# Performance work log

Measured on AMD Instinct MI355X. Metric: run time of the kernel, lower is better.

## Reference

```python
import jax, jax.numpy as jnp
import numpy as np

BN_EPS = 1e-5  # torch BatchNorm1d default


def setup_inputs() -> dict:
    key = jax.random.key(0)
    k = jax.random.split(key, 5)
    B, D, L = 4096, 4096, 4  # batch, width, num layers (3 hidden + 1 output)
    x = jax.random.normal(k[0], (B, D), dtype=jnp.float32)
    # Per-layer Linear weights stored as [L, in, out]; scaled like xavier-ish init.
    W = jax.random.normal(k[1], (L, D, D), dtype=jnp.float32) * (1.0 / np.sqrt(D))
    b = jax.random.normal(k[2], (L, D), dtype=jnp.float32) * 0.01
    gamma = jax.random.uniform(k[3], (L, D), dtype=jnp.float32, minval=0.5, maxval=1.5)
    beta = jax.random.normal(k[4], (L, D), dtype=jnp.float32) * 0.1
    return {"x": x, "W": W, "b": b, "gamma": gamma, "beta": beta}


def _layer(h, W_l, b_l, gamma_l, beta_l):
    # one big GEMM replaces the per-neuron GEMV loop + stack
    h = h @ W_l + b_l  # [B, out]
    # BatchNorm1d, training mode: biased batch stats over the batch dim
    mu = jnp.mean(h, axis=0)
    var = jnp.var(h, axis=0)
    h = (h - mu) * jax.lax.rsqrt(var + BN_EPS) * gamma_l + beta_l
    return jax.nn.relu(h)


def reference(x, W, b, gamma, beta):
    out = x
    for l in range(W.shape[0]):  # small fixed layer count
        out = _layer(out, W[l], b[l], gamma[l], beta[l])
    # nn.Softmax(dim=0): softmax over the batch dimension, as in the original
    return jax.nn.softmax(out, axis=0)
```

## Files before the change

### kernel.cpp

```cpp
#include <hip/hip_runtime.h>
#include <stdint.h>

#define DIMD 4096
#define DIMB 4096
#define NLAYER 4
#define NT (DIMD / 64)

typedef unsigned short u16;
typedef __attribute__((ext_vector_type(4))) float f32x4;
typedef __attribute__((ext_vector_type(8))) __bf16 bf16x8;

__device__ __forceinline__ u16 f2bf(float f) {
    union { float f; uint32_t u; } v; v.f = f;
    return (u16)((v.u + 0x7fffu + ((v.u >> 16) & 1u)) >> 16);
}

__global__ void k_cvt(const float* __restrict__ in, u16* __restrict__ out) {
    int i = (blockIdx.x * 256 + threadIdx.x) * 4;
    float4 v = *reinterpret_cast<const float4*>(in + i);
    ushort4 r;
    r.x = f2bf(v.x); r.y = f2bf(v.y); r.z = f2bf(v.z); r.w = f2bf(v.w);
    *reinterpret_cast<ushort4*>(out + i) = r;
}

__global__ void k_trans(const float* __restrict__ W, u16* __restrict__ Wt) {
    __shared__ float tile[64][65];
    const int t = threadIdx.x;
    const int n0 = blockIdx.x * 64, k0 = blockIdx.y * 64;
    const int kr = t >> 4, c4 = (t & 15) * 4;
    #pragma unroll
    for (int r = 0; r < 4; ++r) {
        float4 v = *reinterpret_cast<const float4*>(W + (size_t)(k0 + kr + r * 16) * DIMD + n0 + c4);
        tile[kr + r * 16][c4 + 0] = v.x;
        tile[kr + r * 16][c4 + 1] = v.y;
        tile[kr + r * 16][c4 + 2] = v.z;
        tile[kr + r * 16][c4 + 3] = v.w;
    }
    __syncthreads();
    const int nr = t >> 4, k4 = (t & 15) * 4;
    #pragma unroll
    for (int r = 0; r < 4; ++r) {
        int n = nr + r * 16;
        ushort4 o;
        o.x = f2bf(tile[k4 + 0][n]);
        o.y = f2bf(tile[k4 + 1][n]);
        o.z = f2bf(tile[k4 + 2][n]);
        o.w = f2bf(tile[k4 + 3][n]);
        *reinterpret_cast<ushort4*>(Wt + (size_t)(n0 + n) * DIMD + k0 + k4) = o;
    }
}

#define GLD(g, l) __builtin_amdgcn_global_load_lds( \
    (__attribute__((address_space(1))) void*)(g),   \
    (__attribute__((address_space(3))) void*)(l), 16, 0, 0)

__global__ __launch_bounds__(512, 2) void k_gemm(
        const u16* __restrict__ A, const u16* __restrict__ Bt,
        const float* __restrict__ bias, float* __restrict__ C,
        float* __restrict__ csum, float* __restrict__ csum2) {
    __shared__ __attribute__((aligned(16))) u16 As[2 * 256 * 64];
    __shared__ __attribute__((aligned(16))) u16 Bs[2 * 256 * 64];
    const int tid = threadIdx.x;
    const int lane = tid & 63, wv = tid >> 6;
    const int wm = wv >> 2, wn = wv & 3;
    const int bm = blockIdx.y, bn = blockIdx.x;
    const int lr = lane & 15, lk = lane >> 4;

    const int r0 = tid >> 3;
    const int cswz = (tid & 7) ^ (r0 & 7);
    const u16* gA = A  + (size_t)(bm * 256 + r0) * DIMD + cswz * 8;
    const u16* gB = Bt + (size_t)(bn * 256 + r0) * DIMD + cswz * 8;

#define STAGE_A(h, t, buf) do { \
    const u16* _s = gA + (size_t)(h) * 128 * DIMD + (size_t)(t) * 64; \
    u16* _d = As + (buf) * 16384 + (h) * 8192 + wv * 512; \
    GLD(_s, _d); GLD(_s + (size_t)64 * DIMD, _d + 4096); \
} while (0)
#define STAGE_B(h, t, buf) do { \
    const u16* _s = gB + (size_t)(h) * 128 * DIMD + (size_t)(t) * 64; \
    u16* _d = Bs + (buf) * 16384 + (h) * 8192 + wv * 512; \
    GLD(_s, _d); GLD(_s + (size_t)64 * DIMD, _d + 4096); \
} while (0)

    int aoff[4][2], boff[2][2];
    #pragma unroll
    for (int mf = 0; mf < 4; ++mf)
        #pragma unroll
        for (int ks = 0; ks < 2; ++ks) {
            int row = wm * 128 + mf * 16 + lr;
            aoff[mf][ks] = row * 64 + ((ks * 4 + lk) ^ (row & 7)) * 8;
        }
    #pragma unroll
    for (int nf = 0; nf < 2; ++nf)
        #pragma unroll
        for (int ks = 0; ks < 2; ++ks) {
            int row = wn * 64 + nf * 16 + lr;
            boff[nf][ks] = row * 64 + ((ks * 4 + lk) ^ (row & 7)) * 8;
        }

    f32x4 acc[8][4] = {};
    bf16x8 a[4][2], b0[2][2], b1[2][2];

    STAGE_B(0, 0, 0); STAGE_B(1, 0, 0); STAGE_A(0, 0, 0); STAGE_A(1, 0, 0);
    STAGE_B(0, 1, 1); STAGE_B(1, 1, 1); STAGE_A(0, 1, 1); STAGE_A(1, 1, 1);
    asm volatile("s_waitcnt vmcnt(8)" ::: "memory");
    __builtin_amdgcn_s_barrier();

    for (int t = 0; t < NT; ++t) {
        const int cur = t & 1;
        const u16* Ab = As + cur * 16384;
        const u16* Bb = Bs + cur * 16384;
        const bool pf = (t + 2 < NT);

        #pragma unroll
        for (int mf = 0; mf < 4; ++mf)
            #pragma unroll
            for (int ks = 0; ks < 2; ++ks)
                a[mf][ks] = *reinterpret_cast<const bf16x8*>(Ab + aoff[mf][ks]);
        #pragma unroll
        for (int nf = 0; nf < 2; ++nf)
            #pragma unroll
            for (int ks = 0; ks < 2; ++ks)
                b0[nf][ks] = *reinterpret_cast<const bf16x8*>(Bb + boff[nf][ks]);
        __builtin_amdgcn_s_barrier();
        asm volatile("s_waitcnt lgkmcnt(0)" ::: "memory");
        __builtin_amdgcn_s_setprio(1);
        #pragma unroll
        for (int mf = 0; mf < 4; ++mf)
            #pragma unroll
            for (int nf = 0; nf < 2; ++nf)
                #pragma unroll
                for (int ks = 0; ks < 2; ++ks)
                    acc[mf][nf] = __builtin_amdgcn_mfma_f32_16x16x32_bf16(
                        a[mf][ks], b0[nf][ks], acc[mf][nf], 0, 0, 0);
        __builtin_amdgcn_s_setprio(0);
        __builtin_amdgcn_s_barrier();

        #pragma unroll
        for (int nf = 0; nf < 2; ++nf)
            #pragma unroll
            for (int ks = 0; ks < 2; ++ks)
                b1[nf][ks] = *reinterpret_cast<const bf16x8*>(Bb + 2048 + boff[nf][ks]);
        __builtin_amdgcn_s_barrier();
        asm volatile("s_waitcnt lgkmcnt(0)" ::: "memory");
        __builtin_amdgcn_s_setprio(1);
        #pragma unroll
        for (int mf = 0; mf < 4; ++mf)
            #pragma unroll
            for (int nf = 0; nf < 2; ++nf)
                #pragma unroll
                for (int ks = 0; ks < 2; ++ks)
                    acc[mf][2 + nf] = __builtin_amdgcn_mfma_f32_16x16x32_bf16(
                        a[mf][ks], b1[nf][ks], acc[mf][2 + nf], 0, 0, 0);
        __builtin_amdgcn_s_setprio(0);
        __builtin_amdgcn_s_barrier();

        #pragma unroll
        for (int mf = 0; mf < 4; ++mf)
            #pragma unroll
            for (int ks = 0; ks < 2; ++ks)
                a[mf][ks] = *reinterpret_cast<const bf16x8*>(Ab + 4096 + aoff[mf][ks]);
        if (pf) { STAGE_B(0, t + 2, cur); STAGE_B(1, t + 2, cur); }
        __builtin_amdgcn_s_barrier();
        asm volatile("s_waitcnt lgkmcnt(0)" ::: "memory");
        __builtin_amdgcn_s_setprio(1);
        #pragma unroll
        for (int mf = 0; mf < 4; ++mf)
            #pragma unroll
            for (int nf = 0; nf < 2; ++nf)
                #pragma unroll
                for (int ks = 0; ks < 2; ++ks)
                    acc[4 + mf][2 + nf] = __builtin_amdgcn_mfma_f32_16x16x32_bf16(
                        a[mf][ks], b1[nf][ks], acc[4 + mf][2 + nf], 0, 0, 0);
        __builtin_amdgcn_s_setprio(0);
        __builtin_amdgcn_s_barrier();

        if (pf) { STAGE_A(0, t + 2, cur); STAGE_A(1, t + 2, cur); }
        __builtin_amdgcn_s_setprio(1);
        #pragma unroll
        for (int mf = 0; mf < 4; ++mf)
            #pragma unroll
            for (int nf = 0; nf < 2; ++nf)
                #pragma unroll
                for (int ks = 0; ks < 2; ++ks)
                    acc[4 + mf][nf] = __builtin_amdgcn_mfma_f32_16x16x32_bf16(
                        a[mf][ks], b0[nf][ks], acc[4 + mf][nf], 0, 0, 0);
        __builtin_amdgcn_s_setprio(0);
        if (pf) asm volatile("s_waitcnt vmcnt(8)" ::: "memory");
        else    asm volatile("s_waitcnt vmcnt(0)" ::: "memory");
        __builtin_amdgcn_s_barrier();
    }

    #pragma unroll
    for (int nh = 0; nh < 2; ++nh)
        #pragma unroll
        for (int nf = 0; nf < 2; ++nf) {
            int n = nh * 2 + nf;
            int col = bn * 256 + wn * 64 + nh * 32 + nf * 16 + lr;
            float bv = bias[col];
            float s1 = 0.f, s2 = 0.f;
            #pragma unroll
            for (int m = 0; m < 8; ++m) {
                int rbase = bm * 256 + wm * 128 + (m >> 2) * 64 + (m & 3) * 16 + lk * 4;
                #pragma unroll
                for (int r = 0; r < 4; ++r) {
                    float v = acc[m][n][r] + bv;
                    C[(size_t)(rbase + r) * DIMD + col] = v;
                    s1 += v; s2 += v * v;
                }
            }
            s1 += __shfl_xor(s1, 16); s1 += __shfl_xor(s1, 32);
            s2 += __shfl_xor(s2, 16); s2 += __shfl_xor(s2, 32);
            if (lk == 0) {
                atomicAdd(&csum[col], s1);
                atomicAdd(&csum2[col], s2);
            }
        }
#undef STAGE_A
#undef STAGE_B
}

__global__ void k_bnfin(float* __restrict__ sum, float* __restrict__ sum2,
                        const float* __restrict__ gamma, const float* __restrict__ beta) {
    int j = blockIdx.x * 256 + threadIdx.x;
    float mu = sum[j] * (1.0f / DIMB);
    float var = sum2[j] * (1.0f / DIMB) - mu * mu;
    float rstd = rsqrtf(var + 1e-5f);
    float s = gamma[j] * rstd;
    sum[j] = s;
    sum2[j] = beta[j] - mu * s;
}

__global__ void k_norm(const float* __restrict__ H, const float* __restrict__ s,
                       const float* __restrict__ t, u16* __restrict__ o) {
    int j = blockIdx.x * 256 + threadIdx.x;
    int i0 = blockIdx.y * 128;
    float sj = s[j], tj = t[j];
    for (int i = i0; i < i0 + 128; ++i) {
        float v = fmaxf(H[(size_t)i * DIMD + j] * sj + tj, 0.0f);
        o[(size_t)i * DIMD + j] = f2bf(v);
    }
}

__global__ void k_normexp(float* __restrict__ H, const float* __restrict__ s,
                          const float* __restrict__ t, float* __restrict__ esum) {
    int j = blockIdx.x * 256 + threadIdx.x;
    int i0 = blockIdx.y * 128;
    float sj = s[j], tj = t[j];
    float acc = 0.f;
    for (int i = i0; i < i0 + 128; ++i) {
        float v = fmaxf(H[(size_t)i * DIMD + j] * sj + tj, 0.0f);
        float e = __expf(v);
        H[(size_t)i * DIMD + j] = e;
        acc += e;
    }
    atomicAdd(&esum[j], acc);
}

__global__ void k_div(float* __restrict__ H, const float* __restrict__ esum) {
    int i = (blockIdx.x * 256 + threadIdx.x) * 4;
    float4 v = *reinterpret_cast<const float4*>(H + i);
    const float4 e = *reinterpret_cast<const float4*>(esum + (i & (DIMD - 1)));
    v.x /= e.x; v.y /= e.y; v.z /= e.z; v.w /= e.w;
    *reinterpret_cast<float4*>(H + i) = v;
}

extern "C" void kernel_launch(void* const* d_in, const int* in_sizes, int n_in,
                              void* d_out, int out_size, void* d_ws, size_t ws_size,
                              hipStream_t stream) {
    (void)in_sizes; (void)n_in; (void)out_size; (void)ws_size;
    const float* x     = (const float*)d_in[0];
    const float* W     = (const float*)d_in[1];
    const float* b     = (const float*)d_in[2];
    const float* gamma = (const float*)d_in[3];
    const float* beta  = (const float*)d_in[4];
    float* out = (float*)d_out;

    char* ws = (char*)d_ws;
    u16*  Abf   = (u16*)ws;
    u16*  Wt    = (u16*)(ws + (size_t)32 * 1024 * 1024);
    float* stats = (float*)(ws + (size_t)64 * 1024 * 1024);
    hipMemsetAsync(stats, 0, (4 * 8192 + 4096) * sizeof(float), stream);

    k_cvt<<<DIMB * DIMD / 1024, 256, 0, stream>>>(x, Abf);

    for (int l = 0; l < NLAYER; ++l) {
        k_trans<<<dim3(64, 64), 256, 0, stream>>>(W + (size_t)l * DIMD * DIMD, Wt);
        float* sum = stats + l * 8192;
        float* sum2 = sum + 4096;
        k_gemm<<<dim3(16, 16), 512, 0, stream>>>(Abf, Wt, b + l * DIMD, out, sum, sum2);
        k_bnfin<<<16, 256, 0, stream>>>(sum, sum2, gamma + l * DIMD, beta + l * DIMD);
        if (l < NLAYER - 1)
            k_norm<<<dim3(16, 32), 256, 0, stream>>>(out, sum, sum2, Abf);
        else
            k_normexp<<<dim3(16, 32), 256, 0, stream>>>(out, sum, sum2, stats + 32768);
    }
    k_div<<<DIMB * DIMD / 1024, 256, 0, stream>>>(out, stats + 32768);
}
```

Measured before the change: 733.7 us.

## Switch GEMM to 32x32x16 MFMA, batch weight transposes, fold BN finalize into norm

The GEMM inner loop now uses 32x32x16 bf16 MFMA instructions instead of 16x16x32. The LDS fragment offsets and the epilogue row mapping are rewritten to match the larger accumulator layout. The intent is fewer MFMA issues and fewer LDS reads per FLOP. All four weight transposes are merged into one 3D launch writing a larger workspace, and the BN finalize kernel is folded into the norm kernels to cut launches. The cost is more workspace memory and a recomputed finalize in every norm block.

```diff
diff --git a/kernel.cpp b/kernel.cpp
--- a/kernel.cpp
+++ b/kernel.cpp
@@ -7,7 +7,7 @@
 #define NT (DIMD / 64)
 
 typedef unsigned short u16;
-typedef __attribute__((ext_vector_type(4))) float f32x4;
+typedef __attribute__((ext_vector_type(16))) float f32x16;
 typedef __attribute__((ext_vector_type(8))) __bf16 bf16x8;
 
 __device__ __forceinline__ u16 f2bf(float f) {
@@ -26,11 +26,12 @@
 __global__ void k_trans(const float* __restrict__ W, u16* __restrict__ Wt) {
     __shared__ float tile[64][65];
     const int t = threadIdx.x;
+    const size_t loff = (size_t)blockIdx.z * DIMD * DIMD;
     const int n0 = blockIdx.x * 64, k0 = blockIdx.y * 64;
     const int kr = t >> 4, c4 = (t & 15) * 4;
     #pragma unroll
     for (int r = 0; r < 4; ++r) {
-        float4 v = *reinterpret_cast<const float4*>(W + (size_t)(k0 + kr + r * 16) * DIMD + n0 + c4);
+        float4 v = *reinterpret_cast<const float4*>(W + loff + (size_t)(k0 + kr + r * 16) * DIMD + n0 + c4);
         tile[kr + r * 16][c4 + 0] = v.x;
         tile[kr + r * 16][c4 + 1] = v.y;
         tile[kr + r * 16][c4 + 2] = v.z;
@@ -46,7 +47,7 @@
         o.y = f2bf(tile[k4 + 1][n]);
         o.z = f2bf(tile[k4 + 2][n]);
         o.w = f2bf(tile[k4 + 3][n]);
-        *reinterpret_cast<ushort4*>(Wt + (size_t)(n0 + n) * DIMD + k0 + k4) = o;
+        *reinterpret_cast<ushort4*>(Wt + loff + (size_t)(n0 + n) * DIMD + k0 + k4) = o;
     }
 }
 
@@ -64,7 +65,7 @@
     const int lane = tid & 63, wv = tid >> 6;
     const int wm = wv >> 2, wn = wv & 3;
     const int bm = blockIdx.y, bn = blockIdx.x;
-    const int lr = lane & 15, lk = lane >> 4;
+    const int lc = lane & 31, lh = lane >> 5;
 
     const int r0 = tid >> 3;
     const int cswz = (tid & 7) ^ (r0 & 7);
@@ -82,24 +83,24 @@
     GLD(_s, _d); GLD(_s + (size_t)64 * DIMD, _d + 4096); \
 } while (0)
 
-    int aoff[4][2], boff[2][2];
+    int aoff[4][4], boff[2][4];
     #pragma unroll
     for (int mf = 0; mf < 4; ++mf)
         #pragma unroll
-        for (int ks = 0; ks < 2; ++ks) {
-            int row = wm * 128 + mf * 16 + lr;
-            aoff[mf][ks] = row * 64 + ((ks * 4 + lk) ^ (row & 7)) * 8;
+        for (int ks = 0; ks < 4; ++ks) {
+            int row = wm * 128 + mf * 32 + lc;
+            aoff[mf][ks] = row * 64 + ((ks * 2 + lh) ^ (row & 7)) * 8;
         }
     #pragma unroll
     for (int nf = 0; nf < 2; ++nf)
         #pragma unroll
-        for (int ks = 0; ks < 2; ++ks) {
-            int row = wn * 64 + nf * 16 + lr;
-            boff[nf][ks] = row * 64 + ((ks * 4 + lk) ^ (row & 7)) * 8;
-        }
-
-    f32x4 acc[8][4] = {};
-    bf16x8 a[4][2], b0[2][2], b1[2][2];
+        for (int ks = 0; ks < 4; ++ks) {
+            int row = wn * 64 + nf * 32 + lc;
+            boff[nf][ks] = row * 64 + ((ks * 2 + lh) ^ (row & 7)) * 8;
+        }
+
+    f32x16 acc[4][2] = {};
+    bf16x8 a[2][4], b0[4], b1[4];
 
     STAGE_B(0, 0, 0); STAGE_B(1, 0, 0); STAGE_A(0, 0, 0); STAGE_A(1, 0, 0);
     STAGE_B(0, 1, 1); STAGE_B(1, 1, 1); STAGE_A(0, 1, 1); STAGE_A(1, 1, 1);
@@ -113,78 +114,66 @@
         const bool pf = (t + 2 < NT);
 
         #pragma unroll
-        for (int mf = 0; mf < 4; ++mf)
-            #pragma unroll
-            for (int ks = 0; ks < 2; ++ks)
+        for (int mf = 0; mf < 2; ++mf)
+            #pragma unroll
+            for (int ks = 0; ks < 4; ++ks)
                 a[mf][ks] = *reinterpret_cast<const bf16x8*>(Ab + aoff[mf][ks]);
         #pragma unroll
-        for (int nf = 0; nf < 2; ++nf)
-            #pragma unroll
-            for (int ks = 0; ks < 2; ++ks)
-                b0[nf][ks] = *reinterpret_cast<const bf16x8*>(Bb + boff[nf][ks]);
+        for (int ks = 0; ks < 4; ++ks)
+            b0[ks] = *reinterpret_cast<const bf16x8*>(Bb + boff[0][ks]);
         __builtin_amdgcn_s_barrier();
         asm volatile("s_waitcnt lgkmcnt(0)" ::: "memory");
         __builtin_amdgcn_s_setprio(1);
         #pragma unroll
-        for (int mf = 0; mf < 4; ++mf)
-            #pragma unroll
-            for (int nf = 0; nf < 2; ++nf)
-                #pragma unroll
-                for (int ks = 0; ks < 2; ++ks)
-                    acc[mf][nf] = __builtin_amdgcn_mfma_f32_16x16x32_bf16(
-                        a[mf][ks], b0[nf][ks], acc[mf][nf], 0, 0, 0);
-        __builtin_amdgcn_s_setprio(0);
-        __builtin_amdgcn_s_barrier();
-
-        #pragma unroll
-        for (int nf = 0; nf < 2; ++nf)
-            #pragma unroll
-            for (int ks = 0; ks < 2; ++ks)
-                b1[nf][ks] = *reinterpret_cast<const bf16x8*>(Bb + 2048 + boff[nf][ks]);
+        for (int ks = 0; ks < 4; ++ks)
+            #pragma unroll
+            for (int mf = 0; mf < 2; ++mf)
+                acc[mf][0] = __builtin_amdgcn_mfma_f32_32x32x16_bf16(
+                    a[mf][ks], b0[ks], acc[mf][0], 0, 0, 0);
+        __builtin_amdgcn_s_setprio(0);
+        __builtin_amdgcn_s_barrier();
+
+        #pragma unroll
+        for (int ks = 0; ks < 4; ++ks)
+            b1[ks] = *reinterpret_cast<const bf16x8*>(Bb + boff[1][ks]);
         __builtin_amdgcn_s_barrier();
         asm volatile("s_waitcnt lgkmcnt(0)" ::: "memory");
         __builtin_amdgcn_s_setprio(1);
         #pragma unroll
-        for (int mf = 0; mf < 4; ++mf)
-            #pragma unroll
-            for (int nf = 0; nf < 2; ++nf)
-                #pragma unroll
-                for (int ks = 0; ks < 2; ++ks)
-                    acc[mf][2 + nf] = __builtin_amdgcn_mfma_f32_16x16x32_bf16(
-                        a[mf][ks], b1[nf][ks], acc[mf][2 + nf], 0, 0, 0);
-        __builtin_amdgcn_s_setprio(0);
-        __builtin_amdgcn_s_barrier();
-
-        #pragma unroll
-        for (int mf = 0; mf < 4; ++mf)
-            #pragma unroll
-            for (int ks = 0; ks < 2; ++ks)
-                a[mf][ks] = *reinterpret_cast<const bf16x8*>(Ab + 4096 + aoff[mf][ks]);
+        for (int ks = 0; ks < 4; ++ks)
+            #pragma unroll
+            for (int mf = 0; mf < 2; ++mf)
+                acc[mf][1] = __builtin_amdgcn_mfma_f32_32x32x16_bf16(
+                    a[mf][ks], b1[ks], acc[mf][1], 0, 0, 0);
+        __builtin_amdgcn_s_setprio(0);
+        __builtin_amdgcn_s_barrier();
+
+        #pragma unroll
+        for (int mf = 0; mf < 2; ++mf)
+            #pragma unroll
+            for (int ks = 0; ks < 4; ++ks)
+                a[mf][ks] = *reinterpret_cast<const bf16x8*>(Ab + aoff[2 + mf][ks]);
         if (pf) { STAGE_B(0, t + 2, cur); STAGE_B(1, t + 2, cur); }
         __builtin_amdgcn_s_barrier();
         asm volatile("s_waitcnt lgkmcnt(0)" ::: "memory");
         __builtin_amdgcn_s_setprio(1);
         #pragma unroll
-        for (int mf = 0; mf < 4; ++mf)
-            #pragma unroll
-            for (int nf = 0; nf < 2; ++nf)
-                #pragma unroll
-                for (int ks = 0; ks < 2; ++ks)
-                    acc[4 + mf][2 + nf] = __builtin_amdgcn_mfma_f32_16x16x32_bf16(
-                        a[mf][ks], b1[nf][ks], acc[4 + mf][2 + nf], 0, 0, 0);
+        for (int ks = 0; ks < 4; ++ks)
+            #pragma unroll
+            for (int mf = 0; mf < 2; ++mf)
+                acc[2 + mf][1] = __builtin_amdgcn_mfma_f32_32x32x16_bf16(
+                    a[mf][ks], b1[ks], acc[2 + mf][1], 0, 0, 0);
         __builtin_amdgcn_s_setprio(0);
         __builtin_amdgcn_s_barrier();
 
         if (pf) { STAGE_A(0, t + 2, cur); STAGE_A(1, t + 2, cur); }
         __builtin_amdgcn_s_setprio(1);
         #pragma unroll
-        for (int mf = 0; mf < 4; ++mf)
-            #pragma unroll
-            for (int nf = 0; nf < 2; ++nf)
-                #pragma unroll
-                for (int ks = 0; ks < 2; ++ks)
-                    acc[4 + mf][nf] = __builtin_amdgcn_mfma_f32_16x16x32_bf16(
-                        a[mf][ks], b0[nf][ks], acc[4 + mf][nf], 0, 0, 0);
+        for (int ks = 0; ks < 4; ++ks)
+            #pragma unroll
+            for (int mf = 0; mf < 2; ++mf)
+                acc[2 + mf][0] = __builtin_amdgcn_mfma_f32_32x32x16_bf16(
+                    a[mf][ks], b0[ks], acc[2 + mf][0], 0, 0, 0);
         __builtin_amdgcn_s_setprio(0);
         if (pf) asm volatile("s_waitcnt vmcnt(8)" ::: "memory");
         else    asm volatile("s_waitcnt vmcnt(0)" ::: "memory");
@@ -192,61 +181,56 @@
     }
 
     #pragma unroll
-    for (int nh = 0; nh < 2; ++nh)
-        #pragma unroll
-        for (int nf = 0; nf < 2; ++nf) {
-            int n = nh * 2 + nf;
-            int col = bn * 256 + wn * 64 + nh * 32 + nf * 16 + lr;
-            float bv = bias[col];
-            float s1 = 0.f, s2 = 0.f;
-            #pragma unroll
-            for (int m = 0; m < 8; ++m) {
-                int rbase = bm * 256 + wm * 128 + (m >> 2) * 64 + (m & 3) * 16 + lk * 4;
-                #pragma unroll
-                for (int r = 0; r < 4; ++r) {
-                    float v = acc[m][n][r] + bv;
-                    C[(size_t)(rbase + r) * DIMD + col] = v;
-                    s1 += v; s2 += v * v;
-                }
+    for (int nf = 0; nf < 2; ++nf) {
+        int col = bn * 256 + wn * 64 + nf * 32 + lc;
+        float bv = bias[col];
+        float s1 = 0.f, s2 = 0.f;
+        #pragma unroll
+        for (int mf = 0; mf < 4; ++mf) {
+            int rbase = bm * 256 + wm * 128 + mf * 32 + lh * 4;
+            #pragma unroll
+            for (int r = 0; r < 16; ++r) {
+                int row = rbase + (r & 3) + 8 * (r >> 2);
+                float v = acc[mf][nf][r] + bv;
+                C[(size_t)row * DIMD + col] = v;
+                s1 += v; s2 += v * v;
             }
-            s1 += __shfl_xor(s1, 16); s1 += __shfl_xor(s1, 32);
-            s2 += __shfl_xor(s2, 16); s2 += __shfl_xor(s2, 32);
-            if (lk == 0) {
-                atomicAdd(&csum[col], s1);
-                atomicAdd(&csum2[col], s2);
-            }
-        }
+        }
+        s1 += __shfl_xor(s1, 32);
+        s2 += __shfl_xor(s2, 32);
+        if (lh == 0) {
+            atomicAdd(&csum[col], s1);
+            atomicAdd(&csum2[col], s2);
+        }
+    }
 #undef STAGE_A
 #undef STAGE_B
 }
 
-__global__ void k_bnfin(float* __restrict__ sum, float* __restrict__ sum2,
-                        const float* __restrict__ gamma, const float* __restrict__ beta) {
+__global__ void k_norm(const float* __restrict__ H, const float* __restrict__ sum,
+                       const float* __restrict__ sum2, const float* __restrict__ gamma,
+                       const float* __restrict__ beta, u16* __restrict__ o) {
     int j = blockIdx.x * 256 + threadIdx.x;
+    int i0 = blockIdx.y * 128;
     float mu = sum[j] * (1.0f / DIMB);
     float var = sum2[j] * (1.0f / DIMB) - mu * mu;
-    float rstd = rsqrtf(var + 1e-5f);
-    float s = gamma[j] * rstd;
-    sum[j] = s;
-    sum2[j] = beta[j] - mu * s;
-}
-
-__global__ void k_norm(const float* __restrict__ H, const float* __restrict__ s,
-                       const float* __restrict__ t, u16* __restrict__ o) {
-    int j = blockIdx.x * 256 + threadIdx.x;
-    int i0 = blockIdx.y * 128;
-    float sj = s[j], tj = t[j];
+    float sj = gamma[j] * rsqrtf(var + 1e-5f);
+    float tj = beta[j] - mu * sj;
     for (int i = i0; i < i0 + 128; ++i) {
         float v = fmaxf(H[(size_t)i * DIMD + j] * sj + tj, 0.0f);
         o[(size_t)i * DIMD + j] = f2bf(v);
     }
 }
 
-__global__ void k_normexp(float* __restrict__ H, const float* __restrict__ s,
-                          const float* __restrict__ t, float* __restrict__ esum) {
+__global__ void k_normexp(float* __restrict__ H, const float* __restrict__ sum,
+                          const float* __restrict__ sum2, const float* __restrict__ gamma,
+                          const float* __restrict__ beta, float* __restrict__ esum) {
     int j = blockIdx.x * 256 + threadIdx.x;
     int i0 = blockIdx.y * 128;
-    float sj = s[j], tj = t[j];
+    float mu = sum[j] * (1.0f / DIMB);
+    float var = sum2[j] * (1.0f / DIMB) - mu * mu;
+    float sj = gamma[j] * rsqrtf(var + 1e-5f);
+    float tj = beta[j] - mu * sj;
     float acc = 0.f;
     for (int i = i0; i < i0 + 128; ++i) {
         float v = fmaxf(H[(size_t)i * DIMD + j] * sj + tj, 0.0f);
@@ -277,23 +261,25 @@
     float* out = (float*)d_out;
 
     char* ws = (char*)d_ws;
-    u16*  Abf   = (u16*)ws;
-    u16*  Wt    = (u16*)(ws + (size_t)32 * 1024 * 1024);
-    float* stats = (float*)(ws + (size_t)64 * 1024 * 1024);
+    u16*  Abf = (u16*)ws;
+    u16*  Wt4 = (u16*)(ws + (size_t)32 * 1024 * 1024);
+    float* stats = (float*)(ws + (size_t)160 * 1024 * 1024);
     hipMemsetAsync(stats, 0, (4 * 8192 + 4096) * sizeof(float), stream);
 
     k_cvt<<<DIMB * DIMD / 1024, 256, 0, stream>>>(x, Abf);
+    k_trans<<<dim3(64, 64, 4), 256, 0, stream>>>(W, Wt4);
 
     for (int l = 0; l < NLAYER; ++l) {
-        k_trans<<<dim3(64, 64), 256, 0, stream>>>(W + (size_t)l * DIMD * DIMD, Wt);
         float* sum = stats + l * 8192;
         float* sum2 = sum + 4096;
-        k_gemm<<<dim3(16, 16), 512, 0, stream>>>(Abf, Wt, b + l * DIMD, out, sum, sum2);
-        k_bnfin<<<16, 256, 0, stream>>>(sum, sum2, gamma + l * DIMD, beta + l * DIMD);
+        k_gemm<<<dim3(16, 16), 512, 0, stream>>>(Abf, Wt4 + (size_t)l * DIMD * DIMD,
+                                                 b + l * DIMD, out, sum, sum2);
         if (l < NLAYER - 1)
-            k_norm<<<dim3(16, 32), 256, 0, stream>>>(out, sum, sum2, Abf);
+            k_norm<<<dim3(16, 32), 256, 0, stream>>>(out, sum, sum2,
+                gamma + l * DIMD, beta + l * DIMD, Abf);
         else
-            k_normexp<<<dim3(16, 32), 256, 0, stream>>>(out, sum, sum2, stats + 32768);
+            k_normexp<<<dim3(16, 32), 256, 0, stream>>>(out, sum, sum2,
+                gamma + l * DIMD, beta + l * DIMD, stats + 32768);
     }
     k_div<<<DIMB * DIMD / 1024, 256, 0, stream>>>(out, stats + 32768);
 }
```

New measurement: 818.8 us. +11.6%, slower.
